# Kernel tuning notes

Measured on AMD Instinct MI355X. Metric: run time of the kernel, lower is better.

The kernel has to match this reference:

```python
import jax, jax.numpy as jnp
import numpy as np

M = 4  # num_modals
EPS = 1e-6


def setup_inputs() -> dict:
    key = jax.random.key(0)
    ks = jax.random.split(key, 12)
    c, h, r, B, n = 768, 3072, 16, 4, 1024
    inp = {
        "x": jax.random.normal(ks[0], (M * B, n, c), jnp.float32),
        "fc1_w": jax.random.normal(ks[1], (h, c), jnp.float32) * 0.02,
        "fc1_b": jax.random.normal(ks[2], (h,), jnp.float32) * 0.02,
        "fc2_w": jax.random.normal(ks[3], (c, h), jnp.float32) * 0.02,
        "fc2_b": jax.random.normal(ks[4], (c,), jnp.float32) * 0.02,
        "a_fc1": jax.random.normal(ks[5], (M, r, c), jnp.float32) * 0.02,
        "b_fc1": jax.random.normal(ks[6], (M, h, r), jnp.float32) * 0.02,
        "a_fc2": jax.random.normal(ks[7], (M, r, h), jnp.float32) * 0.02,
        "b_fc2": jax.random.normal(ks[8], (M, c, r), jnp.float32) * 0.02,
        "gate_w": jax.random.normal(ks[9], (M, M, c), jnp.float32) * 0.02,
        "gate_b": jax.random.normal(ks[10], (M, M), jnp.float32) * 0.02,
        "modality_mask": jax.random.randint(ks[11], (M, B), 0, 2, jnp.int32),
    }
    return inp


def _fused_combine(rw, mask_f, lora):
    # rw: [M,B,n,M] routing softmax; mask_f: [M,B]; lora: [M,B,n,d]
    # per_routing_weights[i,j,t,k] = rw[i,j,t,k] * mask[k,j], renormalized over k
    masked = rw * mask_f.T[None, :, None, :]                      # [M,B,n,M]
    norm = masked / (jnp.sum(masked, axis=-1, keepdims=True) + EPS)
    fused = jnp.einsum("ibnk,kbnd->ibnd", norm, lora)             # combine experts
    return fused * mask_f[:, :, None, None]                       # rows with mask==0 stay zero


def reference(x, fc1_w, fc1_b, fc2_w, fc2_b, a_fc1, b_fc1, a_fc2, b_fc2,
              gate_w, gate_b, modality_mask):
    bs_m, n, c = x.shape
    B = bs_m // M
    xm = x.reshape(M, B, n, c)
    mask_f = modality_mask.astype(x.dtype)                        # [M,B]

    # base fc1
    x1 = (jnp.einsum("ibnc,hc->ibnh", xm, fc1_w) + fc1_b)         # [M,B,n,h]

    # per-modality routing softmax over M experts (computed in fp32 as in torch)
    logits = jnp.einsum("ibnc,iec->ibne", xm, gate_w) + gate_b[:, None, None, :]
    rw = jax.nn.softmax(logits.astype(jnp.float32), axis=-1).astype(x.dtype)

    # HiRA delta for fc1: elementwise(fc1_w, B@A) per modality
    delta1 = fc1_w[None] * jnp.einsum("ihr,irc->ihc", b_fc1, a_fc1)  # [M,h,c]
    lora1 = jnp.einsum("ibnc,ihc->ibnh", xm, delta1)              # [M,B,n,h]

    x1 = x1 + _fused_combine(rw, mask_f, lora1)
    x1 = jax.nn.gelu(x1, approximate=False)                       # mlp.act

    # base fc2
    x2 = jnp.einsum("ibnh,ch->ibnc", x1, fc2_w) + fc2_b           # [M,B,n,c]

    # HiRA delta for fc2
    delta2 = fc2_w[None] * jnp.einsum("icr,irh->ich", b_fc2, a_fc2)  # [M,c,h]
    lora2 = jnp.einsum("ibnh,ich->ibnc", x1, delta2)              # [M,B,n,c]

    x2 = x2 + _fused_combine(rw, mask_f, lora2)
    return x2.reshape(bs_m, n, c)
```

## Files before the change

### kernel.cpp

```cpp
#include <hip/hip_runtime.h>
#include <hip/hip_bf16.h>
#include <math.h>

#define NMOD 4
#define NB 4
#define NTOKN 1024
#define CDIM 768
#define HDIM 3072
#define RDIM 16
#define MROWS (NMOD*NB*NTOKN)
#define RPM (NB*NTOKN)

typedef __bf16 bf16_t;
typedef __bf16 bf16x4 __attribute__((ext_vector_type(4)));
typedef __bf16 bf16x8 __attribute__((ext_vector_type(8)));
typedef float f32x4 __attribute__((ext_vector_type(4)));

__global__ void cvt_kernel(const float* __restrict__ in, bf16_t* __restrict__ out, int n) {
  int i = (blockIdx.x * blockDim.x + threadIdx.x) * 4;
  if (i >= n) return;
  const float4 v = *reinterpret_cast<const float4*>(in + i);
  bf16x4 o;
  o[0] = (bf16_t)v.x; o[1] = (bf16_t)v.y; o[2] = (bf16_t)v.z; o[3] = (bf16_t)v.w;
  *reinterpret_cast<bf16x4*>(out + i) = o;
}

__global__ void delta1_kernel(const float* __restrict__ fc1w, const float* __restrict__ a1,
                              const float* __restrict__ b1, bf16_t* __restrict__ out) {
  int idx = blockIdx.x * blockDim.x + threadIdx.x;
  if (idx >= NMOD*HDIM*CDIM) return;
  int c = idx % CDIM;
  int h = (idx / CDIM) % HDIM;
  int k = idx / (CDIM*HDIM);
  const float* brow = b1 + ((size_t)k*HDIM + h)*RDIM;
  const float* acol = a1 + (size_t)k*RDIM*CDIM + c;
  float s = 0.f;
  #pragma unroll
  for (int r = 0; r < RDIM; ++r) s += brow[r] * acol[r*CDIM];
  out[idx] = (bf16_t)(fc1w[h*CDIM + c] * s);
}

__global__ void delta2_kernel(const float* __restrict__ fc2w, const float* __restrict__ a2,
                              const float* __restrict__ b2, bf16_t* __restrict__ out) {
  int idx = blockIdx.x * blockDim.x + threadIdx.x;
  if (idx >= NMOD*CDIM*HDIM) return;
  int h = idx % HDIM;
  int c = (idx / HDIM) % CDIM;
  int k = idx / (HDIM*CDIM);
  const float* brow = b2 + ((size_t)k*CDIM + c)*RDIM;
  const float* acol = a2 + (size_t)k*RDIM*HDIM + h;
  float s = 0.f;
  #pragma unroll
  for (int r = 0; r < RDIM; ++r) s += brow[r] * acol[r*HDIM];
  out[idx] = (bf16_t)(fc2w[c*HDIM + h] * s);
}

__global__ void gate_kernel(const float* __restrict__ x, const float* __restrict__ gw,
                            const float* __restrict__ gb, const int* __restrict__ mask,
                            float* __restrict__ normw, bf16_t* __restrict__ x_bf) {
  int t = blockIdx.x * 4 + (threadIdx.x >> 6);
  int lane = threadIdx.x & 63;
  int i = t >> 12;
  int b = (t >> 10) & 3;
  const float* xr = x + (size_t)t * CDIM;
  bf16_t* xo = x_bf + (size_t)t * CDIM;
  float acc[NMOD] = {0.f, 0.f, 0.f, 0.f};
  for (int c = lane; c < CDIM; c += 64) {
    float xv = xr[c];
    xo[c] = (bf16_t)xv;
    #pragma unroll
    for (int e = 0; e < NMOD; ++e) acc[e] += xv * gw[(i*NMOD + e)*CDIM + c];
  }
  #pragma unroll
  for (int e = 0; e < NMOD; ++e) {
    float v = acc[e];
    #pragma unroll
    for (int off = 32; off > 0; off >>= 1) v += __shfl_xor(v, off);
    acc[e] = v;
  }
  if (lane == 0) {
    float lg[NMOD], mx = -1e30f;
    #pragma unroll
    for (int e = 0; e < NMOD; ++e) { lg[e] = acc[e] + gb[i*NMOD + e]; mx = fmaxf(mx, lg[e]); }
    float s = 0.f;
    #pragma unroll
    for (int e = 0; e < NMOD; ++e) { lg[e] = expf(lg[e] - mx); s += lg[e]; }
    float inv = 1.f / s;
    float num[NMOD], den = 0.f;
    #pragma unroll
    for (int k = 0; k < NMOD; ++k) {
      float mk = (float)mask[k*NB + b];
      num[k] = lg[k] * inv * mk;
      den += num[k];
    }
    float mi = (float)mask[i*NB + b];
    float scale = mi / (den + 1e-6f);
    #pragma unroll
    for (int k = 0; k < NMOD; ++k) normw[(size_t)t*4 + k] = num[k] * scale;
  }
}

#define BMT 128
#define BNT 128
#define BKT 64

__device__ __forceinline__ void gload_lds16(const bf16_t* g, bf16_t* l) {
  __builtin_amdgcn_global_load_lds((const __attribute__((address_space(1))) void*)g,
                                   (__attribute__((address_space(3))) void*)l, 16, 0, 0);
}
#define MFMA_BF16 __builtin_amdgcn_mfma_f32_16x16x32_bf16

__global__ __launch_bounds__(256, 4)
void gemm_kernel(const bf16_t* __restrict__ A, const bf16_t* __restrict__ W0,
                 const bf16_t* __restrict__ WL, const float* __restrict__ bias,
                 const int* __restrict__ mask,
                 bf16_t* __restrict__ outB, bf16_t* __restrict__ outL,
                 int K, int N, int P, int modStride, int rowOff, int posOff) {
  __shared__ __align__(16) bf16_t As[BMT * BKT];
  __shared__ __align__(16) bf16_t Bs[BNT * BKT];

  const int tid  = threadIdx.x;
  const int lane = tid & 63;
  const int wv   = tid >> 6;
  const int wr   = wv >> 1, wc = wv & 1;
  const int row0 = blockIdx.x * BMT;
  const int col0 = blockIdx.y * BNT;
  const bool lora = (blockIdx.z != 0);

  const int mod = row0 / P;
  if (lora) {
    const int bb = (posOff + (row0 % P)) >> 10;
    if (mask[mod*NB + bb] == 0) return;
  }
  const int gArow0 = mod * modStride + rowOff + (row0 % P);
  const bf16_t* Wp = lora ? (WL + (size_t)mod * N * K) : W0;

  const int ldr = tid >> 3;
  const int ssl = ((tid & 7) ^ (ldr & 7)) * 8;
  const bf16_t* Ag = A  + (size_t)(gArow0 + ldr) * K + ssl;
  const bf16_t* Wg = Wp + (size_t)(col0   + ldr) * K + ssl;

  const int fr  = lane & 15;
  const int hi  = lane >> 4;
  const int sk0 = ((hi)     ^ (fr & 7)) * 8;
  const int sk1 = ((4 + hi) ^ (fr & 7)) * 8;

  f32x4 acc[4][4];
  #pragma unroll
  for (int i = 0; i < 4; ++i)
    #pragma unroll
    for (int j = 0; j < 4; ++j) acc[i][j] = (f32x4){0.f, 0.f, 0.f, 0.f};

  for (int k0 = 0; k0 < K; k0 += BKT) {
    __syncthreads();
    #pragma unroll
    for (int j = 0; j < 4; ++j)
      gload_lds16(Ag + (size_t)(j*32) * K + k0, &As[tid*8 + j*2048]);
    #pragma unroll
    for (int j = 0; j < 4; ++j)
      gload_lds16(Wg + (size_t)(j*32) * K + k0, &Bs[tid*8 + j*2048]);
    __syncthreads();

    #pragma unroll
    for (int kk = 0; kk < 2; ++kk) {
      const int sk = (kk == 0) ? sk0 : sk1;
      bf16x8 af[4], bfr[4];
      #pragma unroll
      for (int mi = 0; mi < 4; ++mi)
        af[mi] = *reinterpret_cast<const bf16x8*>(&As[(wr*64 + mi*16 + fr)*BKT + sk]);
      #pragma unroll
      for (int ni = 0; ni < 4; ++ni)
        bfr[ni] = *reinterpret_cast<const bf16x8*>(&Bs[(wc*64 + ni*16 + fr)*BKT + sk]);
      #pragma unroll
      for (int mi = 0; mi < 4; ++mi)
        #pragma unroll
        for (int ni = 0; ni < 4; ++ni)
          acc[mi][ni] = MFMA_BF16(af[mi], bfr[ni], acc[mi][ni], 0, 0, 0);
    }
  }

  bf16_t* outp = lora ? outL : outB;
  #pragma unroll
  for (int mi = 0; mi < 4; ++mi) {
    #pragma unroll
    for (int ni = 0; ni < 4; ++ni) {
      const int colg = col0 + wc*64 + ni*16 + fr;
      float bv = 0.f;
      if (!lora) bv = bias[colg];
      #pragma unroll
      for (int rg = 0; rg < 4; ++rg) {
        const int rowg = row0 + wr*64 + mi*16 + hi*4 + rg;
        outp[(size_t)rowg * N + colg] = (bf16_t)(acc[mi][ni][rg] + bv);
      }
    }
  }
}

__global__ void combine1_kernel(bf16_t* __restrict__ base1, const bf16_t* __restrict__ L1,
                                const float* __restrict__ normw, const int* __restrict__ mask,
                                int P, int chunkOff) {
  int idx = blockIdx.x * blockDim.x + threadIdx.x;
  if (idx >= P * (HDIM/8)) return;
  int h0 = (idx % (HDIM/8)) * 8;
  int p  = idx / (HDIM/8);
  const int b = (chunkOff + p) >> 10;
  float lv[4][8];
  #pragma unroll
  for (int k = 0; k < 4; ++k) {
    if (mask[k*NB + b] != 0) {
      bf16x8 v = *reinterpret_cast<const bf16x8*>(&L1[((size_t)(k*P + p))*HDIM + h0]);
      #pragma unroll
      for (int j = 0; j < 8; ++j) lv[k][j] = (float)v[j];
    } else {
      #pragma unroll
      for (int j = 0; j < 8; ++j) lv[k][j] = 0.f;
    }
  }
  #pragma unroll
  for (int i = 0; i < 4; ++i) {
    size_t ro = ((size_t)(i*P + p))*HDIM + h0;
    const float* nw = normw + ((size_t)(i*RPM + chunkOff + p))*4;
    float n0 = nw[0], n1 = nw[1], n2 = nw[2], n3 = nw[3];
    bf16x8 bv = *reinterpret_cast<const bf16x8*>(&base1[ro]);
    bf16x8 ov;
    #pragma unroll
    for (int j = 0; j < 8; ++j) {
      float v = (float)bv[j] + n0*lv[0][j] + n1*lv[1][j] + n2*lv[2][j] + n3*lv[3][j];
      float g = 0.5f * v * (1.f + erff(v * 0.70710678118654752f));
      ov[j] = (bf16_t)g;
    }
    *reinterpret_cast<bf16x8*>(&base1[ro]) = ov;
  }
}

__global__ void combine2_kernel(const bf16_t* __restrict__ base2, const bf16_t* __restrict__ L2,
                                const float* __restrict__ normw, const int* __restrict__ mask,
                                float* __restrict__ out, int P, int chunkOff) {
  int idx = blockIdx.x * blockDim.x + threadIdx.x;
  if (idx >= P * (CDIM/8)) return;
  int c0 = (idx % (CDIM/8)) * 8;
  int p  = idx / (CDIM/8);
  const int b = (chunkOff + p) >> 10;
  float lv[4][8];
  #pragma unroll
  for (int k = 0; k < 4; ++k) {
    if (mask[k*NB + b] != 0) {
      bf16x8 v = *reinterpret_cast<const bf16x8*>(&L2[((size_t)(k*P + p))*CDIM + c0]);
      #pragma unroll
      for (int j = 0; j < 8; ++j) lv[k][j] = (float)v[j];
    } else {
      #pragma unroll
      for (int j = 0; j < 8; ++j) lv[k][j] = 0.f;
    }
  }
  #pragma unroll
  for (int i = 0; i < 4; ++i) {
    int grow = i*RPM + chunkOff + p;
    const float* nw = normw + (size_t)grow*4;
    float n0 = nw[0], n1 = nw[1], n2 = nw[2], n3 = nw[3];
    bf16x8 bv = *reinterpret_cast<const bf16x8*>(&base2[((size_t)(i*P + p))*CDIM + c0]);
    float o[8];
    #pragma unroll
    for (int j = 0; j < 8; ++j)
      o[j] = (float)bv[j] + n0*lv[0][j] + n1*lv[1][j] + n2*lv[2][j] + n3*lv[3][j];
    float4* op = reinterpret_cast<float4*>(out + (size_t)grow*CDIM + c0);
    op[0] = make_float4(o[0], o[1], o[2], o[3]);
    op[1] = make_float4(o[4], o[5], o[6], o[7]);
  }
}

extern "C" void kernel_launch(void* const* d_in, const int* in_sizes, int n_in,
                              void* d_out, int out_size, void* d_ws, size_t ws_size,
                              hipStream_t stream) {
  (void)in_sizes; (void)n_in; (void)out_size;
  const float* x    = (const float*)d_in[0];
  const float* fc1w = (const float*)d_in[1];
  const float* fc1b = (const float*)d_in[2];
  const float* fc2w = (const float*)d_in[3];
  const float* fc2b = (const float*)d_in[4];
  const float* a1   = (const float*)d_in[5];
  const float* b1   = (const float*)d_in[6];
  const float* a2   = (const float*)d_in[7];
  const float* b2   = (const float*)d_in[8];
  const float* gw   = (const float*)d_in[9];
  const float* gb   = (const float*)d_in[10];
  const int*   mask = (const int*)d_in[11];
  float* out = (float*)d_out;

  char* ws = (char*)d_ws;
  size_t off = 0;
  auto carve = [&](size_t bytes) -> char* {
    char* p = ws + off; off += (bytes + 255) & ~(size_t)255; return p;
  };
  bf16_t* x_bf  = (bf16_t*)carve((size_t)MROWS*CDIM*2);
  bf16_t* w1_bf = (bf16_t*)carve((size_t)HDIM*CDIM*2);
  bf16_t* w2_bf = (bf16_t*)carve((size_t)CDIM*HDIM*2);
  bf16_t* d1_bf = (bf16_t*)carve((size_t)NMOD*HDIM*CDIM*2);
  bf16_t* d2_bf = (bf16_t*)carve((size_t)NMOD*CDIM*HDIM*2);
  float*  normw = (float*)carve((size_t)MROWS*4*4);
  const size_t fixedBytes = off;

  int P = RPM;
  while (P > 128 && fixedBytes + (size_t)61440*P + 4096 > ws_size) P >>= 1;
  const int NCH = RPM / P;

  bf16_t* base1 = (bf16_t*)carve((size_t)NMOD*P*HDIM*2);
  bf16_t* L1    = (bf16_t*)carve((size_t)NMOD*P*HDIM*2);
  bf16_t* base2 = (bf16_t*)carve((size_t)NMOD*P*CDIM*2);
  bf16_t* L2    = (bf16_t*)carve((size_t)NMOD*P*CDIM*2);

  cvt_kernel<<<HDIM*CDIM/1024, 256, 0, stream>>>(fc1w, w1_bf, HDIM*CDIM);
  cvt_kernel<<<CDIM*HDIM/1024, 256, 0, stream>>>(fc2w, w2_bf, CDIM*HDIM);
  delta1_kernel<<<NMOD*HDIM*CDIM/256, 256, 0, stream>>>(fc1w, a1, b1, d1_bf);
  delta2_kernel<<<NMOD*CDIM*HDIM/256, 256, 0, stream>>>(fc2w, a2, b2, d2_bf);
  gate_kernel<<<MROWS/4, 256, 0, stream>>>(x, gw, gb, mask, normw, x_bf);

  for (int g = 0; g < NCH; ++g) {
    const int chunkOff = g * P;
    gemm_kernel<<<dim3(NMOD*P/BMT, HDIM/BNT, 2), 256, 0, stream>>>(
        x_bf, w1_bf, d1_bf, fc1b, mask, base1, L1, CDIM, HDIM, P, RPM, chunkOff, chunkOff);
    combine1_kernel<<<(P*(HDIM/8) + 255)/256, 256, 0, stream>>>(base1, L1, normw, mask, P, chunkOff);
    gemm_kernel<<<dim3(NMOD*P/BMT, CDIM/BNT, 2), 256, 0, stream>>>(
        base1, w2_bf, d2_bf, fc2b, mask, base2, L2, HDIM, CDIM, P, P, 0, chunkOff);
    combine2_kernel<<<(P*(CDIM/8) + 255)/256, 256, 0, stream>>>(base2, L2, normw, mask, out, P, chunkOff);
  }
}
```

Measured before the change: 454.2 us.

## Fuse base and LoRA GEMMs to share A tile; fold weight cast into delta

The GEMM kernel now computes the base and per-modality delta products in the same block. The A tile is loaded into LDS once and feeds two accumulator sets, instead of launching a second grid slice that reloads A. The standalone weight-cast kernels are removed, and the bf16 weight copies are written by the delta kernels when k==0. Workspace is shrunk by aliasing L1 with base2/L2, which may allow larger chunks. The cost is double the accumulator registers and more LDS, so occupancy is lowered to 2 waves per SIMD.

```diff
diff --git a/kernel.cpp b/kernel.cpp
--- a/kernel.cpp
+++ b/kernel.cpp
@@ -16,17 +16,9 @@
 typedef __bf16 bf16x8 __attribute__((ext_vector_type(8)));
 typedef float f32x4 __attribute__((ext_vector_type(4)));
 
-__global__ void cvt_kernel(const float* __restrict__ in, bf16_t* __restrict__ out, int n) {
-  int i = (blockIdx.x * blockDim.x + threadIdx.x) * 4;
-  if (i >= n) return;
-  const float4 v = *reinterpret_cast<const float4*>(in + i);
-  bf16x4 o;
-  o[0] = (bf16_t)v.x; o[1] = (bf16_t)v.y; o[2] = (bf16_t)v.z; o[3] = (bf16_t)v.w;
-  *reinterpret_cast<bf16x4*>(out + i) = o;
-}
-
 __global__ void delta1_kernel(const float* __restrict__ fc1w, const float* __restrict__ a1,
-                              const float* __restrict__ b1, bf16_t* __restrict__ out) {
+                              const float* __restrict__ b1, bf16_t* __restrict__ out,
+                              bf16_t* __restrict__ w_bf) {
   int idx = blockIdx.x * blockDim.x + threadIdx.x;
   if (idx >= NMOD*HDIM*CDIM) return;
   int c = idx % CDIM;
@@ -37,11 +29,14 @@
   float s = 0.f;
   #pragma unroll
   for (int r = 0; r < RDIM; ++r) s += brow[r] * acol[r*CDIM];
-  out[idx] = (bf16_t)(fc1w[h*CDIM + c] * s);
+  const float wv = fc1w[h*CDIM + c];
+  out[idx] = (bf16_t)(wv * s);
+  if (k == 0) w_bf[h*CDIM + c] = (bf16_t)wv;
 }
 
 __global__ void delta2_kernel(const float* __restrict__ fc2w, const float* __restrict__ a2,
-                              const float* __restrict__ b2, bf16_t* __restrict__ out) {
+                              const float* __restrict__ b2, bf16_t* __restrict__ out,
+                              bf16_t* __restrict__ w_bf) {
   int idx = blockIdx.x * blockDim.x + threadIdx.x;
   if (idx >= NMOD*CDIM*HDIM) return;
   int h = idx % HDIM;
@@ -52,7 +47,9 @@
   float s = 0.f;
   #pragma unroll
   for (int r = 0; r < RDIM; ++r) s += brow[r] * acol[r*HDIM];
-  out[idx] = (bf16_t)(fc2w[c*HDIM + h] * s);
+  const float wv = fc2w[c*HDIM + h];
+  out[idx] = (bf16_t)(wv * s);
+  if (k == 0) w_bf[c*HDIM + h] = (bf16_t)wv;
 }
 
 __global__ void gate_kernel(const float* __restrict__ x, const float* __restrict__ gw,
@@ -110,14 +107,15 @@
 }
 #define MFMA_BF16 __builtin_amdgcn_mfma_f32_16x16x32_bf16
 
-__global__ __launch_bounds__(256, 4)
+__global__ __launch_bounds__(256, 2)
 void gemm_kernel(const bf16_t* __restrict__ A, const bf16_t* __restrict__ W0,
                  const bf16_t* __restrict__ WL, const float* __restrict__ bias,
                  const int* __restrict__ mask,
                  bf16_t* __restrict__ outB, bf16_t* __restrict__ outL,
                  int K, int N, int P, int modStride, int rowOff, int posOff) {
-  __shared__ __align__(16) bf16_t As[BMT * BKT];
-  __shared__ __align__(16) bf16_t Bs[BNT * BKT];
+  __shared__ __align__(16) bf16_t As [BMT * BKT];
+  __shared__ __align__(16) bf16_t Bs0[BNT * BKT];
+  __shared__ __align__(16) bf16_t Bs1[BNT * BKT];
 
   const int tid  = threadIdx.x;
   const int lane = tid & 63;
@@ -125,72 +123,101 @@
   const int wr   = wv >> 1, wc = wv & 1;
   const int row0 = blockIdx.x * BMT;
   const int col0 = blockIdx.y * BNT;
-  const bool lora = (blockIdx.z != 0);
 
   const int mod = row0 / P;
-  if (lora) {
-    const int bb = (posOff + (row0 % P)) >> 10;
-    if (mask[mod*NB + bb] == 0) return;
-  }
+  const int bb  = (posOff + (row0 % P)) >> 10;
+  const bool doL = (mask[mod*NB + bb] != 0);
   const int gArow0 = mod * modStride + rowOff + (row0 % P);
-  const bf16_t* Wp = lora ? (WL + (size_t)mod * N * K) : W0;
+  const bf16_t* WpL = WL + (size_t)mod * N * K;
 
   const int ldr = tid >> 3;
   const int ssl = ((tid & 7) ^ (ldr & 7)) * 8;
-  const bf16_t* Ag = A  + (size_t)(gArow0 + ldr) * K + ssl;
-  const bf16_t* Wg = Wp + (size_t)(col0   + ldr) * K + ssl;
+  const bf16_t* Ag  = A   + (size_t)(gArow0 + ldr) * K + ssl;
+  const bf16_t* W0g = W0  + (size_t)(col0   + ldr) * K + ssl;
+  const bf16_t* W1g = WpL + (size_t)(col0   + ldr) * K + ssl;
 
   const int fr  = lane & 15;
   const int hi  = lane >> 4;
   const int sk0 = ((hi)     ^ (fr & 7)) * 8;
   const int sk1 = ((4 + hi) ^ (fr & 7)) * 8;
 
-  f32x4 acc[4][4];
+  f32x4 acc0[4][4], acc1[4][4];
   #pragma unroll
   for (int i = 0; i < 4; ++i)
     #pragma unroll
-    for (int j = 0; j < 4; ++j) acc[i][j] = (f32x4){0.f, 0.f, 0.f, 0.f};
+    for (int j = 0; j < 4; ++j) {
+      acc0[i][j] = (f32x4){0.f, 0.f, 0.f, 0.f};
+      acc1[i][j] = (f32x4){0.f, 0.f, 0.f, 0.f};
+    }
 
   for (int k0 = 0; k0 < K; k0 += BKT) {
     __syncthreads();
     #pragma unroll
     for (int j = 0; j < 4; ++j)
-      gload_lds16(Ag + (size_t)(j*32) * K + k0, &As[tid*8 + j*2048]);
+      gload_lds16(Ag  + (size_t)(j*32) * K + k0, &As [tid*8 + j*2048]);
     #pragma unroll
     for (int j = 0; j < 4; ++j)
-      gload_lds16(Wg + (size_t)(j*32) * K + k0, &Bs[tid*8 + j*2048]);
+      gload_lds16(W0g + (size_t)(j*32) * K + k0, &Bs0[tid*8 + j*2048]);
+    if (doL) {
+      #pragma unroll
+      for (int j = 0; j < 4; ++j)
+        gload_lds16(W1g + (size_t)(j*32) * K + k0, &Bs1[tid*8 + j*2048]);
+    }
     __syncthreads();
 
     #pragma unroll
     for (int kk = 0; kk < 2; ++kk) {
       const int sk = (kk == 0) ? sk0 : sk1;
-      bf16x8 af[4], bfr[4];
+      bf16x8 af[4], b0[4];
       #pragma unroll
       for (int mi = 0; mi < 4; ++mi)
         af[mi] = *reinterpret_cast<const bf16x8*>(&As[(wr*64 + mi*16 + fr)*BKT + sk]);
       #pragma unroll
       for (int ni = 0; ni < 4; ++ni)
-        bfr[ni] = *reinterpret_cast<const bf16x8*>(&Bs[(wc*64 + ni*16 + fr)*BKT + sk]);
+        b0[ni] = *reinterpret_cast<const bf16x8*>(&Bs0[(wc*64 + ni*16 + fr)*BKT + sk]);
       #pragma unroll
       for (int mi = 0; mi < 4; ++mi)
         #pragma unroll
         for (int ni = 0; ni < 4; ++ni)
-          acc[mi][ni] = MFMA_BF16(af[mi], bfr[ni], acc[mi][ni], 0, 0, 0);
-    }
-  }
-
-  bf16_t* outp = lora ? outL : outB;
+          acc0[mi][ni] = MFMA_BF16(af[mi], b0[ni], acc0[mi][ni], 0, 0, 0);
+      if (doL) {
+        bf16x8 b1[4];
+        #pragma unroll
+        for (int ni = 0; ni < 4; ++ni)
+          b1[ni] = *reinterpret_cast<const bf16x8*>(&Bs1[(wc*64 + ni*16 + fr)*BKT + sk]);
+        #pragma unroll
+        for (int mi = 0; mi < 4; ++mi)
+          #pragma unroll
+          for (int ni = 0; ni < 4; ++ni)
+            acc1[mi][ni] = MFMA_BF16(af[mi], b1[ni], acc1[mi][ni], 0, 0, 0);
+      }
+    }
+  }
+
   #pragma unroll
   for (int mi = 0; mi < 4; ++mi) {
     #pragma unroll
     for (int ni = 0; ni < 4; ++ni) {
       const int colg = col0 + wc*64 + ni*16 + fr;
-      float bv = 0.f;
-      if (!lora) bv = bias[colg];
+      const float bv = bias[colg];
       #pragma unroll
       for (int rg = 0; rg < 4; ++rg) {
         const int rowg = row0 + wr*64 + mi*16 + hi*4 + rg;
-        outp[(size_t)rowg * N + colg] = (bf16_t)(acc[mi][ni][rg] + bv);
+        outB[(size_t)rowg * N + colg] = (bf16_t)(acc0[mi][ni][rg] + bv);
+      }
+    }
+  }
+  if (doL) {
+    #pragma unroll
+    for (int mi = 0; mi < 4; ++mi) {
+      #pragma unroll
+      for (int ni = 0; ni < 4; ++ni) {
+        const int colg = col0 + wc*64 + ni*16 + fr;
+        #pragma unroll
+        for (int rg = 0; rg < 4; ++rg) {
+          const int rowg = row0 + wr*64 + mi*16 + hi*4 + rg;
+          outL[(size_t)rowg * N + colg] = (bf16_t)(acc1[mi][ni][rg]);
+        }
       }
     }
   }
@@ -301,26 +328,25 @@
   const size_t fixedBytes = off;
 
   int P = RPM;
-  while (P > 128 && fixedBytes + (size_t)61440*P + 4096 > ws_size) P >>= 1;
+  while (P > 128 && fixedBytes + (size_t)49152*P + 4096 > ws_size) P >>= 1;
   const int NCH = RPM / P;
 
   bf16_t* base1 = (bf16_t*)carve((size_t)NMOD*P*HDIM*2);
-  bf16_t* L1    = (bf16_t*)carve((size_t)NMOD*P*HDIM*2);
-  bf16_t* base2 = (bf16_t*)carve((size_t)NMOD*P*CDIM*2);
-  bf16_t* L2    = (bf16_t*)carve((size_t)NMOD*P*CDIM*2);
-
-  cvt_kernel<<<HDIM*CDIM/1024, 256, 0, stream>>>(fc1w, w1_bf, HDIM*CDIM);
-  cvt_kernel<<<CDIM*HDIM/1024, 256, 0, stream>>>(fc2w, w2_bf, CDIM*HDIM);
-  delta1_kernel<<<NMOD*HDIM*CDIM/256, 256, 0, stream>>>(fc1w, a1, b1, d1_bf);
-  delta2_kernel<<<NMOD*CDIM*HDIM/256, 256, 0, stream>>>(fc2w, a2, b2, d2_bf);
+  bf16_t* Lbuf  = (bf16_t*)carve((size_t)NMOD*P*HDIM*2);
+  bf16_t* L1    = Lbuf;
+  bf16_t* base2 = Lbuf;
+  bf16_t* L2    = Lbuf + (size_t)NMOD*P*CDIM;
+
+  delta1_kernel<<<NMOD*HDIM*CDIM/256, 256, 0, stream>>>(fc1w, a1, b1, d1_bf, w1_bf);
+  delta2_kernel<<<NMOD*CDIM*HDIM/256, 256, 0, stream>>>(fc2w, a2, b2, d2_bf, w2_bf);
   gate_kernel<<<MROWS/4, 256, 0, stream>>>(x, gw, gb, mask, normw, x_bf);
 
   for (int g = 0; g < NCH; ++g) {
     const int chunkOff = g * P;
-    gemm_kernel<<<dim3(NMOD*P/BMT, HDIM/BNT, 2), 256, 0, stream>>>(
+    gemm_kernel<<<dim3(NMOD*P/BMT, HDIM/BNT), 256, 0, stream>>>(
         x_bf, w1_bf, d1_bf, fc1b, mask, base1, L1, CDIM, HDIM, P, RPM, chunkOff, chunkOff);
     combine1_kernel<<<(P*(HDIM/8) + 255)/256, 256, 0, stream>>>(base1, L1, normw, mask, P, chunkOff);
-    gemm_kernel<<<dim3(NMOD*P/BMT, CDIM/BNT, 2), 256, 0, stream>>>(
+    gemm_kernel<<<dim3(NMOD*P/BMT, CDIM/BNT), 256, 0, stream>>>(
         base1, w2_bf, d2_bf, fc2b, mask, base2, L2, HDIM, CDIM, P, P, 0, chunkOff);
     combine2_kernel<<<(P*(CDIM/8) + 255)/256, 256, 0, stream>>>(base2, L2, normw, mask, out, P, chunkOff);
   }
```

Result: no change. 458.5 us (+1.0%).
